# Performance work log

Measured on AMD Instinct MI355X. Metric: run time of the kernel, lower is better.

The kernel has to match this reference:

```python
import jax, jax.numpy as jnp
import numpy as np

B, N, D, DN, F, NUM_F, O, H = 8, 4096, 256, 128, 128, 1024, 8, 1024
EPS = 1e-5

def setup_inputs() -> dict:
    key = jax.random.key(0)
    ks = jax.random.split(key, 10)
    s = 0.02
    x = jax.random.normal(ks[0], (B, N, D), dtype=jnp.float32)
    ctx = jax.random.normal(ks[1], (B, DN), dtype=jnp.float32)
    idx = jax.random.randint(ks[2], (F,), 0, NUM_F, dtype=jnp.int64)
    cond_w = jax.random.normal(ks[3], (DN, 2 * D), dtype=jnp.float32) * s
    cond_b = jnp.zeros((2 * D,), dtype=jnp.float32)
    ffn_w_in = jax.random.normal(ks[4], (D, 2 * H), dtype=jnp.float32) * s
    ffn_b_in = jnp.zeros((2 * H,), dtype=jnp.float32)
    ffn_w_out = jax.random.normal(ks[5], (H, D), dtype=jnp.float32) * s
    ffn_b_out = jnp.zeros((D,), dtype=jnp.float32)
    emb = jax.random.normal(ks[6], (NUM_F, D * O), dtype=jnp.float32) * s
    return {"x": x, "ctx": ctx, "idx": idx, "cond_w": cond_w, "cond_b": cond_b,
            "ffn_w_in": ffn_w_in, "ffn_b_in": ffn_b_in,
            "ffn_w_out": ffn_w_out, "ffn_b_out": ffn_b_out, "emb": emb}

def reference(x, ctx, idx, cond_w, cond_b, ffn_w_in, ffn_b_in, ffn_w_out, ffn_b_out, emb):
    # Conditional LayerNorm: normalize over last dim, FiLM-style modulation from ctx
    mu = jnp.mean(x, axis=-1, keepdims=True)
    var = jnp.mean((x - mu) ** 2, axis=-1, keepdims=True)
    h = (x - mu) * jax.lax.rsqrt(var + EPS)                      # [B,N,D]
    ss = ctx @ cond_w + cond_b                                   # [B,2D]
    scale, shift = jnp.split(ss, 2, axis=-1)                     # [B,D] each
    h = h * (1.0 + scale[:, None, :]) + shift[:, None, :]
    # Gated FFN: in-proj -> (gelu(gate) * value) -> out-proj
    uv = h @ ffn_w_in + ffn_b_in                                 # [B,N,2H]
    u, v = jnp.split(uv, 2, axis=-1)
    y = (jax.nn.gelu(u) * v) @ ffn_w_out + ffn_b_out             # [B,N,D]
    # Embedding-generated per-feature output weights, then batched contraction
    w = emb[idx].reshape(F, D, O)                                # gather [F,D,O]
    out = jnp.einsum('bnd,fdo->bnfo', y, w)                      # [B,N,F,O]
    return out
```

## Files before the change

kernel.cpp:

```cpp
#include <hip/hip_runtime.h>
#include <cstdint>
#include <cstddef>

#define M_TOT 32768
#define D_    256
#define DN_   128
#define TWO_D 512
#define H_    1024
#define TWO_H 2048

typedef unsigned short ushort_t;
typedef __attribute__((ext_vector_type(8))) short bf16x8;
typedef __attribute__((ext_vector_type(4))) float f32x4;

__device__ __forceinline__ ushort_t f2bf(float f) {
  union { float f; uint32_t i; } v; v.f = f;
  uint32_t r = v.i + 0x7fffu + ((v.i >> 16) & 1u);
  return (ushort_t)(r >> 16);
}

__device__ __forceinline__ void async_ld16(const void* g, void* l) {
  __builtin_amdgcn_global_load_lds(
      (const __attribute__((address_space(1))) void*)g,
      (__attribute__((address_space(3))) void*)l, 16, 0, 0);
}

__global__ __launch_bounds__(256) void cond_ss_kernel(
    const float* __restrict__ ctx, const float* __restrict__ cond_w,
    const float* __restrict__ cond_b, float* __restrict__ ss) {
  int j = blockIdx.x * 256 + threadIdx.x;
  int b = j >> 9, col = j & 511;
  float acc = cond_b[col];
  for (int k = 0; k < DN_; ++k)
    acc += ctx[b * DN_ + k] * cond_w[k * TWO_D + col];
  ss[j] = acc;
}

__global__ __launch_bounds__(256) void transpose_f32_bf16_kernel(
    const float* __restrict__ in, ushort_t* __restrict__ out, int R, int C) {
  __shared__ float T[64 * 65];
  int ctiles = C >> 6;
  int bi = blockIdx.x / ctiles, bj = blockIdx.x % ctiles;
  int r0 = bi * 64, c0 = bj * 64;
  int tid = threadIdx.x;
#pragma unroll
  for (int it = 0; it < 16; ++it) {
    int idx = it * 256 + tid;
    int r = idx >> 6, c = idx & 63;
    T[r * 65 + c] = in[(size_t)(r0 + r) * C + c0 + c];
  }
  __syncthreads();
#pragma unroll
  for (int it = 0; it < 8; ++it) {
    int idx = it * 256 + tid;
    int a = idx >> 5;
    int b = (idx & 31) * 2;
    uint32_t pk = (uint32_t)f2bf(T[b * 65 + a]) |
                  ((uint32_t)f2bf(T[(b + 1) * 65 + a]) << 16);
    *(uint32_t*)&out[(size_t)(c0 + a) * R + r0 + b] = pk;
  }
}

__global__ __launch_bounds__(256) void gather_emb_kernel(
    const float* __restrict__ emb, const int* __restrict__ idx,
    ushort_t* __restrict__ W2T) {
  int f = blockIdx.x;
  bool looks64 = (idx[1] == 0) & (idx[3] == 0) & (idx[5] == 0) & (idx[7] == 0);
  int fi = looks64 ? idx[2 * f] : idx[f];
  const float* src = emb + (size_t)fi * 2048;
  int o = threadIdx.x >> 5, d0 = (threadIdx.x & 31) * 8;
  ushort_t buf[8];
#pragma unroll
  for (int k = 0; k < 8; ++k) buf[k] = f2bf(src[(d0 + k) * 8 + o]);
  *(bf16x8*)&W2T[(size_t)(f * 8 + o) * 256 + d0] = *(bf16x8*)buf;
}

__global__ __launch_bounds__(256) void ln_film_kernel(
    const float* __restrict__ x, const float* __restrict__ ss,
    ushort_t* __restrict__ h) {
  int row = blockIdx.x * 4 + (threadIdx.x >> 6);
  int lane = threadIdx.x & 63;
  int b = row >> 12;
  const float* xr = x + (size_t)row * D_;
  float4 pk = *(const float4*)(xr + lane * 4);
  float f0 = pk.x, f1 = pk.y, f2 = pk.z, f3 = pk.w;
  float s = f0 + f1 + f2 + f3;
  float q = f0 * f0 + f1 * f1 + f2 * f2 + f3 * f3;
#pragma unroll
  for (int off = 32; off > 0; off >>= 1) {
    s += __shfl_xor(s, off, 64);
    q += __shfl_xor(q, off, 64);
  }
  float mean = s * (1.0f / 256.0f);
  float var = q * (1.0f / 256.0f) - mean * mean;
  float rs = rsqrtf(var + 1e-5f);
  int d = lane * 4;
  const float* ssb = ss + b * TWO_D;
  float o0 = (f0 - mean) * rs * (1.0f + ssb[d + 0]) + ssb[256 + d + 0];
  float o1 = (f1 - mean) * rs * (1.0f + ssb[d + 1]) + ssb[256 + d + 1];
  float o2 = (f2 - mean) * rs * (1.0f + ssb[d + 2]) + ssb[256 + d + 2];
  float o3 = (f3 - mean) * rs * (1.0f + ssb[d + 3]) + ssb[256 + d + 3];
  uint2 st;
  st.x = (uint32_t)f2bf(o0) | ((uint32_t)f2bf(o1) << 16);
  st.y = (uint32_t)f2bf(o2) | ((uint32_t)f2bf(o3) << 16);
  *(uint2*)(h + (size_t)row * D_ + lane * 4) = st;
}

__global__ __launch_bounds__(256, 2) void ffn_fused_kernel(
    const ushort_t* __restrict__ h,
    const ushort_t* __restrict__ WinT,
    const float* __restrict__ bin,
    const ushort_t* __restrict__ WoutT,
    const float* __restrict__ bout,
    ushort_t* __restrict__ y) {
  __shared__ ushort_t Ah[64 * 256];
  __shared__ ushort_t Sh[64 * 264];
  __shared__ ushort_t Gs[64 * 72];
  const int tid = threadIdx.x, lane = tid & 63, wave = tid >> 6;
  const int r = lane >> 2, q = lane & 3;
  const int l15 = lane & 15, l4 = lane >> 4;
  const int m0 = blockIdx.x * 64;
  const int fragoff = l15 * 32 + l4 * 8;

  for (int t = wave; t < 32; t += 4) {
    int rt = t & 3, kc = t >> 2;
    async_ld16(h + (size_t)(m0 + rt * 16 + r) * 256 + kc * 32 + q * 8, &Ah[t * 512]);
  }

  f32x4 yac[16] = {};

  for (int j = 0; j < 16; ++j) {
    f32x4 uac[4] = {}, vac[4] = {};
#pragma unroll
    for (int s = 0; s < 2; ++s) {
      __syncthreads();
      for (int t = wave; t < 16; t += 4) {
        int rt = t & 3, kc = t >> 2;
        size_t grow = (size_t)(j * 64 + rt * 16 + r);
        async_ld16(WinT + grow * 256 + s * 128 + kc * 32 + q * 8, &Sh[t * 512]);
        async_ld16(WinT + (grow + 1024) * 256 + s * 128 + kc * 32 + q * 8, &Sh[(16 + t) * 512]);
      }
      __syncthreads();
#pragma unroll
      for (int ks = 0; ks < 4; ++ks) {
        bf16x8 af = *(const bf16x8*)&Ah[((s * 4 + ks) * 4 + wave) * 512 + fragoff];
#pragma unroll
        for (int jt = 0; jt < 4; ++jt) {
          bf16x8 bu = *(const bf16x8*)&Sh[(ks * 4 + jt) * 512 + fragoff];
          bf16x8 bv = *(const bf16x8*)&Sh[(16 + ks * 4 + jt) * 512 + fragoff];
          uac[jt] = __builtin_amdgcn_mfma_f32_16x16x32_bf16(af, bu, uac[jt], 0, 0, 0);
          vac[jt] = __builtin_amdgcn_mfma_f32_16x16x32_bf16(af, bv, vac[jt], 0, 0, 0);
        }
      }
    }
#pragma unroll
    for (int jt = 0; jt < 4; ++jt) {
      int col = jt * 16 + l15;
      float bub = bin[j * 64 + col];
      float bvb = bin[1024 + j * 64 + col];
#pragma unroll
      for (int rr = 0; rr < 4; ++rr) {
        float u = uac[jt][rr] + bub;
        float v = vac[jt][rr] + bvb;
        float t = 0.7978845608028654f * (u + 0.044715f * u * u * u);
        float e = __expf(2.0f * t);
        float th = 1.0f - 2.0f / (e + 1.0f);
        float gl = 0.5f * u * (1.0f + th);
        Gs[(wave * 16 + l4 * 4 + rr) * 72 + col] = f2bf(gl * v);
      }
    }
    __syncthreads();
    for (int t = wave; t < 32; t += 4) {
      int nt = t & 15, s2 = t >> 4;
      async_ld16(WoutT + (size_t)(nt * 16 + r) * 1024 + j * 64 + s2 * 32 + q * 8, &Sh[t * 512]);
    }
    __syncthreads();
#pragma unroll
    for (int s2 = 0; s2 < 2; ++s2) {
      bf16x8 gf = *(const bf16x8*)&Gs[(wave * 16 + l15) * 72 + s2 * 32 + l4 * 8];
#pragma unroll
      for (int nt = 0; nt < 16; ++nt) {
        bf16x8 bw = *(const bf16x8*)&Sh[(s2 * 16 + nt) * 512 + fragoff];
        yac[nt] = __builtin_amdgcn_mfma_f32_16x16x32_bf16(gf, bw, yac[nt], 0, 0, 0);
      }
    }
  }
  __syncthreads();
#pragma unroll
  for (int nt = 0; nt < 16; ++nt) {
    int col = nt * 16 + l15;
    float bb = bout[col];
#pragma unroll
    for (int rr = 0; rr < 4; ++rr)
      Sh[(wave * 16 + l4 * 4 + rr) * 264 + col] = f2bf(yac[nt][rr] + bb);
  }
  __syncthreads();
#pragma unroll
  for (int it = 0; it < 8; ++it) {
    int id = it * 256 + tid;
    int rr = id >> 5, cc = id & 31;
    bf16x8 vv = *(const bf16x8*)&Sh[rr * 264 + cc * 8];
    *(bf16x8*)&y[(size_t)(m0 + rr) * 256 + cc * 8] = vv;
  }
}

__global__ __launch_bounds__(256, 2) void gemm_out_kernel(
    const ushort_t* __restrict__ A, const ushort_t* __restrict__ BT,
    float* __restrict__ C) {
  __shared__ ushort_t As[128 * 64];
  __shared__ ushort_t Bs[128 * 64];
  __shared__ float Cs[64 * 132];
  const int tid = threadIdx.x, lane = tid & 63, wave = tid >> 6;
  const int wm = wave >> 1, wn = wave & 1;
  const int m0 = blockIdx.x * 128, n0 = blockIdx.y * 128;
  const int r = lane >> 2, q = lane & 3;
  const int l15 = lane & 15, l4 = lane >> 4;
  const int fragoff = l15 * 32 + l4 * 8;
  const int N = 1024, K = 256;
  f32x4 acc[4][4] = {};
  for (int k0 = 0; k0 < K; k0 += 64) {
    for (int t = wave; t < 16; t += 4) {
      int rt = t >> 1, ks = t & 1;
      async_ld16(A + (size_t)(m0 + rt * 16 + r) * K + k0 + ks * 32 + q * 8, &As[t * 512]);
      async_ld16(BT + (size_t)(n0 + rt * 16 + r) * K + k0 + ks * 32 + q * 8, &Bs[t * 512]);
    }
    __syncthreads();
#pragma unroll
    for (int ks = 0; ks < 2; ++ks) {
      bf16x8 a[4], b[4];
#pragma unroll
      for (int i = 0; i < 4; ++i)
        a[i] = *(const bf16x8*)&As[((wm * 4 + i) * 2 + ks) * 512 + fragoff];
#pragma unroll
      for (int jt = 0; jt < 4; ++jt)
        b[jt] = *(const bf16x8*)&Bs[((wn * 4 + jt) * 2 + ks) * 512 + fragoff];
#pragma unroll
      for (int i = 0; i < 4; ++i)
#pragma unroll
        for (int jt = 0; jt < 4; ++jt)
          acc[i][jt] = __builtin_amdgcn_mfma_f32_16x16x32_bf16(a[i], b[jt], acc[i][jt], 0, 0, 0);
    }
    __syncthreads();
  }
#pragma unroll
  for (int p = 0; p < 2; ++p) {
    __syncthreads();
    if (wm == p) {
#pragma unroll
      for (int jt = 0; jt < 4; ++jt) {
        int col = wn * 64 + jt * 16 + l15;
#pragma unroll
        for (int i = 0; i < 4; ++i) {
          int rl = i * 16 + (l4 << 2);
#pragma unroll
          for (int rr = 0; rr < 4; ++rr)
            Cs[(rl + rr) * 132 + col] = acc[i][jt][rr];
        }
      }
    }
    __syncthreads();
#pragma unroll
    for (int it = 0; it < 8; ++it) {
      int t = it * 256 + tid;
      int rr = t >> 5, c = (t & 31) * 4;
      float4 v = *(const float4*)&Cs[rr * 132 + c];
      *(float4*)&C[(size_t)(m0 + p * 64 + rr) * N + n0 + c] = v;
    }
  }
}

extern "C" void kernel_launch(void* const* d_in, const int* in_sizes, int n_in,
                              void* d_out, int out_size, void* d_ws, size_t ws_size,
                              hipStream_t stream) {
  const float* x      = (const float*)d_in[0];
  const float* ctx    = (const float*)d_in[1];
  const int*   idx    = (const int*)d_in[2];
  const float* cond_w = (const float*)d_in[3];
  const float* cond_b = (const float*)d_in[4];
  const float* w_in   = (const float*)d_in[5];
  const float* b_in   = (const float*)d_in[6];
  const float* w_out  = (const float*)d_in[7];
  const float* b_out  = (const float*)d_in[8];
  const float* emb    = (const float*)d_in[9];

  char* w = (char*)d_ws;
  float* ss = (float*)w;           w += (size_t)8 * TWO_D * 4;
  ushort_t* h = (ushort_t*)w;      w += (size_t)M_TOT * D_ * 2;
  ushort_t* y = (ushort_t*)w;      w += (size_t)M_TOT * D_ * 2;
  ushort_t* WinT = (ushort_t*)w;   w += (size_t)TWO_H * D_ * 2;
  ushort_t* WoutT = (ushort_t*)w;  w += (size_t)D_ * H_ * 2;
  ushort_t* W2T = (ushort_t*)w;    w += (size_t)H_ * D_ * 2;

  cond_ss_kernel<<<16, 256, 0, stream>>>(ctx, cond_w, cond_b, ss);
  transpose_f32_bf16_kernel<<<(D_ / 64) * (TWO_H / 64), 256, 0, stream>>>(w_in, WinT, D_, TWO_H);
  transpose_f32_bf16_kernel<<<(H_ / 64) * (D_ / 64), 256, 0, stream>>>(w_out, WoutT, H_, D_);
  gather_emb_kernel<<<128, 256, 0, stream>>>(emb, idx, W2T);
  ln_film_kernel<<<M_TOT / 4, 256, 0, stream>>>(x, ss, h);
  ffn_fused_kernel<<<M_TOT / 64, 256, 0, stream>>>(h, WinT, b_in, WoutT, b_out, y);
  gemm_out_kernel<<<dim3(M_TOT / 128, H_ / 128), 256, 0, stream>>>(y, W2T, (float*)d_out);
}
```

Baseline: 306.9 us.

## Double-buffer FFN weight tiles in LDS and keep activations in registers

```diff
diff --git a/kernel.cpp b/kernel.cpp
--- a/kernel.cpp
+++ b/kernel.cpp
@@ -113,8 +113,7 @@
     const ushort_t* __restrict__ WoutT,
     const float* __restrict__ bout,
     ushort_t* __restrict__ y) {
-  __shared__ ushort_t Ah[64 * 256];
-  __shared__ ushort_t Sh[64 * 264];
+  __shared__ ushort_t Sh[2][16384];
   __shared__ ushort_t Gs[64 * 72];
   const int tid = threadIdx.x, lane = tid & 63, wave = tid >> 6;
   const int r = lane >> 2, q = lane & 3;
@@ -122,35 +121,94 @@
   const int m0 = blockIdx.x * 64;
   const int fragoff = l15 * 32 + l4 * 8;
 
-  for (int t = wave; t < 32; t += 4) {
-    int rt = t & 3, kc = t >> 2;
-    async_ld16(h + (size_t)(m0 + rt * 16 + r) * 256 + kc * 32 + q * 8, &Ah[t * 512]);
+  const char* winp  = (const char*)WinT  + (wave * 16 + r) * 512 + q * 16;
+  const char* woutp = (const char*)WoutT + (size_t)wave * 32768 + r * 2048 + q * 16;
+
+  const ushort_t* hp = h + (size_t)(m0 + wave * 16 + l15) * 256 + l4 * 8;
+  bf16x8 a_reg[8];
+#pragma unroll
+  for (int kc = 0; kc < 8; ++kc) a_reg[kc] = *(const bf16x8*)(hp + kc * 32);
+
+#pragma unroll
+  for (int i = 0; i < 4; ++i) {
+    int t = i * 4 + wave;
+    async_ld16(winp + i * 64,          &Sh[0][t * 512]);
+    async_ld16(winp + i * 64 + 524288, &Sh[0][(16 + t) * 512]);
   }
 
   f32x4 yac[16] = {};
+  int pb = 0;
 
   for (int j = 0; j < 16; ++j) {
+    const int jb = j * 32768;
     f32x4 uac[4] = {}, vac[4] = {};
-#pragma unroll
-    for (int s = 0; s < 2; ++s) {
-      __syncthreads();
-      for (int t = wave; t < 16; t += 4) {
-        int rt = t & 3, kc = t >> 2;
-        size_t grow = (size_t)(j * 64 + rt * 16 + r);
-        async_ld16(WinT + grow * 256 + s * 128 + kc * 32 + q * 8, &Sh[t * 512]);
-        async_ld16(WinT + (grow + 1024) * 256 + s * 128 + kc * 32 + q * 8, &Sh[(16 + t) * 512]);
-      }
-      __syncthreads();
+
+    asm volatile("s_waitcnt vmcnt(0)" ::: "memory");
+    __builtin_amdgcn_s_barrier();
+    asm volatile("" ::: "memory");
+    {
+      ushort_t* nxt = Sh[pb ^ 1];
+#pragma unroll
+      for (int i = 0; i < 4; ++i) {
+        int t = i * 4 + wave;
+        async_ld16(winp + jb + 256 + i * 64,          &nxt[t * 512]);
+        async_ld16(winp + jb + 256 + i * 64 + 524288, &nxt[(16 + t) * 512]);
+      }
+      const ushort_t* cur = Sh[pb];
+      __builtin_amdgcn_s_setprio(1);
 #pragma unroll
       for (int ks = 0; ks < 4; ++ks) {
-        bf16x8 af = *(const bf16x8*)&Ah[((s * 4 + ks) * 4 + wave) * 512 + fragoff];
+        bf16x8 af = a_reg[ks];
 #pragma unroll
         for (int jt = 0; jt < 4; ++jt) {
-          bf16x8 bu = *(const bf16x8*)&Sh[(ks * 4 + jt) * 512 + fragoff];
-          bf16x8 bv = *(const bf16x8*)&Sh[(16 + ks * 4 + jt) * 512 + fragoff];
+          bf16x8 bu = *(const bf16x8*)&cur[(ks * 4 + jt) * 512 + fragoff];
+          bf16x8 bv = *(const bf16x8*)&cur[(16 + ks * 4 + jt) * 512 + fragoff];
           uac[jt] = __builtin_amdgcn_mfma_f32_16x16x32_bf16(af, bu, uac[jt], 0, 0, 0);
           vac[jt] = __builtin_amdgcn_mfma_f32_16x16x32_bf16(af, bv, vac[jt], 0, 0, 0);
         }
+      }
+      __builtin_amdgcn_s_setprio(0);
+    }
+    pb ^= 1;
+
+    asm volatile("s_waitcnt vmcnt(0)" ::: "memory");
+    __builtin_amdgcn_s_barrier();
+    asm volatile("" ::: "memory");
+    {
+      ushort_t* nxt = Sh[pb ^ 1];
+#pragma unroll
+      for (int i = 0; i < 4; ++i) {
+        int t = i * 4 + wave;
+        async_ld16(woutp + (size_t)i * 131072 + j * 128,      &nxt[t * 512]);
+        async_ld16(woutp + (size_t)i * 131072 + j * 128 + 64, &nxt[(16 + t) * 512]);
+      }
+      const ushort_t* cur = Sh[pb];
+      __builtin_amdgcn_s_setprio(1);
+#pragma unroll
+      for (int ks = 0; ks < 4; ++ks) {
+        bf16x8 af = a_reg[4 + ks];
+#pragma unroll
+        for (int jt = 0; jt < 4; ++jt) {
+          bf16x8 bu = *(const bf16x8*)&cur[(ks * 4 + jt) * 512 + fragoff];
+          bf16x8 bv = *(const bf16x8*)&cur[(16 + ks * 4 + jt) * 512 + fragoff];
+          uac[jt] = __builtin_amdgcn_mfma_f32_16x16x32_bf16(af, bu, uac[jt], 0, 0, 0);
+          vac[jt] = __builtin_amdgcn_mfma_f32_16x16x32_bf16(af, bv, vac[jt], 0, 0, 0);
+        }
+      }
+      __builtin_amdgcn_s_setprio(0);
+    }
+    pb ^= 1;
+
+    asm volatile("s_waitcnt vmcnt(0)" ::: "memory");
+    __builtin_amdgcn_s_barrier();
+    asm volatile("" ::: "memory");
+    if (j < 15) {
+      ushort_t* nxt = Sh[pb ^ 1];
+#pragma unroll
+      for (int i = 0; i < 4; ++i) {
+        int t = i * 4 + wave;
+        async_ld16(winp + jb + 32768 + i * 64,          &nxt[t * 512]);
+        async_ld16(winp + jb + 32768 + i * 64 + 524288, &nxt[(16 + t) * 512]);
       }
     }
 #pragma unroll
@@ -169,37 +227,43 @@
         Gs[(wave * 16 + l4 * 4 + rr) * 72 + col] = f2bf(gl * v);
       }
     }
-    __syncthreads();
-    for (int t = wave; t < 32; t += 4) {
-      int nt = t & 15, s2 = t >> 4;
-      async_ld16(WoutT + (size_t)(nt * 16 + r) * 1024 + j * 64 + s2 * 32 + q * 8, &Sh[t * 512]);
-    }
-    __syncthreads();
-#pragma unroll
-    for (int s2 = 0; s2 < 2; ++s2) {
-      bf16x8 gf = *(const bf16x8*)&Gs[(wave * 16 + l15) * 72 + s2 * 32 + l4 * 8];
-#pragma unroll
-      for (int nt = 0; nt < 16; ++nt) {
-        bf16x8 bw = *(const bf16x8*)&Sh[(s2 * 16 + nt) * 512 + fragoff];
-        yac[nt] = __builtin_amdgcn_mfma_f32_16x16x32_bf16(gf, bw, yac[nt], 0, 0, 0);
-      }
-    }
-  }
-  __syncthreads();
+    {
+      const ushort_t* cur = Sh[pb];
+#pragma unroll
+      for (int s2 = 0; s2 < 2; ++s2) {
+        bf16x8 gf = *(const bf16x8*)&Gs[(wave * 16 + l15) * 72 + s2 * 32 + l4 * 8];
+        __builtin_amdgcn_s_setprio(1);
+#pragma unroll
+        for (int nt = 0; nt < 16; ++nt) {
+          bf16x8 bw = *(const bf16x8*)&cur[(s2 * 16 + nt) * 512 + fragoff];
+          yac[nt] = __builtin_amdgcn_mfma_f32_16x16x32_bf16(gf, bw, yac[nt], 0, 0, 0);
+        }
+        __builtin_amdgcn_s_setprio(0);
+      }
+    }
+    pb ^= 1;
+  }
+
+  asm volatile("s_waitcnt vmcnt(0)" ::: "memory");
+  __builtin_amdgcn_s_barrier();
+  asm volatile("" ::: "memory");
+  ushort_t* E = &Sh[0][0];
 #pragma unroll
   for (int nt = 0; nt < 16; ++nt) {
     int col = nt * 16 + l15;
     float bb = bout[col];
 #pragma unroll
     for (int rr = 0; rr < 4; ++rr)
-      Sh[(wave * 16 + l4 * 4 + rr) * 264 + col] = f2bf(yac[nt][rr] + bb);
-  }
-  __syncthreads();
+      E[(wave * 16 + l4 * 4 + rr) * 264 + col] = f2bf(yac[nt][rr] + bb);
+  }
+  asm volatile("s_waitcnt lgkmcnt(0)" ::: "memory");
+  __builtin_amdgcn_s_barrier();
+  asm volatile("" ::: "memory");
 #pragma unroll
   for (int it = 0; it < 8; ++it) {
     int id = it * 256 + tid;
     int rr = id >> 5, cc = id & 31;
-    bf16x8 vv = *(const bf16x8*)&Sh[rr * 264 + cc * 8];
+    bf16x8 vv = *(const bf16x8*)&E[rr * 264 + cc * 8];
     *(bf16x8*)&y[(size_t)(m0 + rr) * 256 + cc * 8] = vv;
   }
 }
```

Result: faster. 299.1 us (-2.6%).

## Pipeline fused FFN with triple-buffered LDS, register-resident A and swizzled layout

Applied to the files above, without the earlier changes.

```diff
diff --git a/kernel.cpp b/kernel.cpp
--- a/kernel.cpp
+++ b/kernel.cpp
@@ -113,95 +113,172 @@
     const ushort_t* __restrict__ WoutT,
     const float* __restrict__ bout,
     ushort_t* __restrict__ y) {
-  __shared__ ushort_t Ah[64 * 256];
-  __shared__ ushort_t Sh[64 * 264];
+  __shared__ ushort_t S3[3][8192];
   __shared__ ushort_t Gs[64 * 72];
+  __shared__ float Lbin[2048];
   const int tid = threadIdx.x, lane = tid & 63, wave = tid >> 6;
+  const int wm = wave >> 1, wn = wave & 1;
   const int r = lane >> 2, q = lane & 3;
+  const int qs = q ^ ((r >> 1) & 3);
   const int l15 = lane & 15, l4 = lane >> 4;
   const int m0 = blockIdx.x * 64;
-  const int fragoff = l15 * 32 + l4 * 8;
-
-  for (int t = wave; t < 32; t += 4) {
-    int rt = t & 3, kc = t >> 2;
-    async_ld16(h + (size_t)(m0 + rt * 16 + r) * 256 + kc * 32 + q * 8, &Ah[t * 512]);
-  }
-
-  f32x4 yac[16] = {};
+  const int fragoff = l15 * 32 + (l4 ^ ((l15 >> 1) & 3)) * 8;
+
+  const char* winb  = (const char*)WinT  + r * 512 + qs * 16;
+  const char* woutb = (const char*)WoutT + r * 2048 + qs * 16;
+
+  const ushort_t* hp = h + (size_t)(m0 + wm * 32 + l15) * 256 + l4 * 8;
+  bf16x8 a_reg[2][8];
+#pragma unroll
+  for (int rt = 0; rt < 2; ++rt)
+#pragma unroll
+    for (int kc = 0; kc < 8; ++kc)
+      a_reg[rt][kc] = *(const bf16x8*)(hp + rt * 4096 + kc * 32);
+
+#pragma unroll
+  for (int i = 0; i < 2; ++i)
+    async_ld16((const char*)bin + (wave * 2 + i) * 1024 + lane * 16,
+               (char*)Lbin + (wave * 2 + i) * 1024);
+
+  auto stage_in = [&](ushort_t* dst, int jrow, int k0e) {
+#pragma unroll
+    for (int i = 0; i < 4; ++i) {
+      int tt = i * 4 + wave;
+      int vv = tt >> 3, t7 = tt & 7;
+      int ks = t7 >> 2, cc = t7 & 3;
+      async_ld16(winb + (size_t)vv * 524288 + jrow * 32768 + cc * 8192 +
+                     k0e * 2 + ks * 64,
+                 &dst[tt * 512]);
+    }
+  };
+  auto stage_wout = [&](ushort_t* dst, int jrow, int s2) {
+#pragma unroll
+    for (int i = 0; i < 4; ++i) {
+      int tt = i * 4 + wave;
+      async_ld16(woutb + (size_t)tt * 32768 + jrow * 128 + s2 * 64,
+                 &dst[tt * 512]);
+    }
+  };
+
+  stage_in(S3[0], 0, 0);
+  stage_in(S3[1], 0, 64);
+
+  f32x4 yac[2][8] = {};
+
+#define ENTRY4()                                        \
+  asm volatile("s_waitcnt vmcnt(4)" ::: "memory");      \
+  __builtin_amdgcn_s_barrier();                         \
+  asm volatile("" ::: "memory");
+#define ENTRY4L()                                                  \
+  asm volatile("s_waitcnt vmcnt(4) lgkmcnt(0)" ::: "memory");      \
+  __builtin_amdgcn_s_barrier();                                    \
+  asm volatile("" ::: "memory");
+
+#define MFMA_IN(buf, p_)                                                      \
+  {                                                                           \
+    const ushort_t* cur_ = (buf);                                             \
+    __builtin_amdgcn_s_setprio(1);                                            \
+    _Pragma("unroll")                                                         \
+    for (int ks = 0; ks < 2; ++ks) {                                          \
+      _Pragma("unroll")                                                       \
+      for (int jj = 0; jj < 2; ++jj) {                                        \
+        int tt = ks * 4 + wn * 2 + jj;                                        \
+        bf16x8 bu = *(const bf16x8*)&cur_[tt * 512 + fragoff];                \
+        bf16x8 bv = *(const bf16x8*)&cur_[(8 + tt) * 512 + fragoff];          \
+        uac[0][jj] = __builtin_amdgcn_mfma_f32_16x16x32_bf16(a_reg[0][(p_)*2+ks], bu, uac[0][jj], 0, 0, 0); \
+        uac[1][jj] = __builtin_amdgcn_mfma_f32_16x16x32_bf16(a_reg[1][(p_)*2+ks], bu, uac[1][jj], 0, 0, 0); \
+        vac[0][jj] = __builtin_amdgcn_mfma_f32_16x16x32_bf16(a_reg[0][(p_)*2+ks], bv, vac[0][jj], 0, 0, 0); \
+        vac[1][jj] = __builtin_amdgcn_mfma_f32_16x16x32_bf16(a_reg[1][(p_)*2+ks], bv, vac[1][jj], 0, 0, 0); \
+      }                                                                       \
+    }                                                                         \
+    __builtin_amdgcn_s_setprio(0);                                            \
+  }
+
+#define MFMA_OUT(buf, s2_)                                                    \
+  {                                                                           \
+    const ushort_t* cur_ = (buf);                                             \
+    bf16x8 gf0 = *(const bf16x8*)&Gs[(wm * 32 + l15) * 72 + (s2_) * 32 + l4 * 8];      \
+    bf16x8 gf1 = *(const bf16x8*)&Gs[(wm * 32 + 16 + l15) * 72 + (s2_) * 32 + l4 * 8]; \
+    __builtin_amdgcn_s_setprio(1);                                            \
+    _Pragma("unroll")                                                         \
+    for (int nt8 = 0; nt8 < 8; ++nt8) {                                       \
+      bf16x8 bw = *(const bf16x8*)&cur_[(wn * 8 + nt8) * 512 + fragoff];      \
+      yac[0][nt8] = __builtin_amdgcn_mfma_f32_16x16x32_bf16(gf0, bw, yac[0][nt8], 0, 0, 0); \
+      yac[1][nt8] = __builtin_amdgcn_mfma_f32_16x16x32_bf16(gf1, bw, yac[1][nt8], 0, 0, 0); \
+    }                                                                         \
+    __builtin_amdgcn_s_setprio(0);                                            \
+  }
 
   for (int j = 0; j < 16; ++j) {
-    f32x4 uac[4] = {}, vac[4] = {};
-#pragma unroll
-    for (int s = 0; s < 2; ++s) {
-      __syncthreads();
-      for (int t = wave; t < 16; t += 4) {
-        int rt = t & 3, kc = t >> 2;
-        size_t grow = (size_t)(j * 64 + rt * 16 + r);
-        async_ld16(WinT + grow * 256 + s * 128 + kc * 32 + q * 8, &Sh[t * 512]);
-        async_ld16(WinT + (grow + 1024) * 256 + s * 128 + kc * 32 + q * 8, &Sh[(16 + t) * 512]);
-      }
-      __syncthreads();
-#pragma unroll
-      for (int ks = 0; ks < 4; ++ks) {
-        bf16x8 af = *(const bf16x8*)&Ah[((s * 4 + ks) * 4 + wave) * 512 + fragoff];
-#pragma unroll
-        for (int jt = 0; jt < 4; ++jt) {
-          bf16x8 bu = *(const bf16x8*)&Sh[(ks * 4 + jt) * 512 + fragoff];
-          bf16x8 bv = *(const bf16x8*)&Sh[(16 + ks * 4 + jt) * 512 + fragoff];
-          uac[jt] = __builtin_amdgcn_mfma_f32_16x16x32_bf16(af, bu, uac[jt], 0, 0, 0);
-          vac[jt] = __builtin_amdgcn_mfma_f32_16x16x32_bf16(af, bv, vac[jt], 0, 0, 0);
+    const int jn = (j + 1) & 15;
+    f32x4 uac[2][2] = {}, vac[2][2] = {};
+
+    ENTRY4(); stage_in(S3[2], j, 128);  MFMA_IN(S3[0], 0);
+    ENTRY4(); stage_in(S3[0], j, 192);  MFMA_IN(S3[1], 1);
+    ENTRY4(); stage_wout(S3[1], j, 0);  MFMA_IN(S3[2], 2);
+    ENTRY4(); stage_wout(S3[2], j, 1);  MFMA_IN(S3[0], 3);
+
+#pragma unroll
+    for (int jj = 0; jj < 2; ++jj) {
+      int gcol = wn * 32 + jj * 16 + l15;
+      float bub = Lbin[j * 64 + gcol];
+      float bvb = Lbin[1024 + j * 64 + gcol];
+#pragma unroll
+      for (int rt = 0; rt < 2; ++rt) {
+#pragma unroll
+        for (int rr = 0; rr < 4; ++rr) {
+          float u = uac[rt][jj][rr] + bub;
+          float v = vac[rt][jj][rr] + bvb;
+          float t = 0.7978845608028654f * (u + 0.044715f * u * u * u);
+          float e = __expf(2.0f * t);
+          float th = 1.0f - 2.0f / (e + 1.0f);
+          float gl = 0.5f * u * (1.0f + th);
+          Gs[(wm * 32 + rt * 16 + l4 * 4 + rr) * 72 + gcol] = f2bf(gl * v);
         }
       }
     }
-#pragma unroll
-    for (int jt = 0; jt < 4; ++jt) {
-      int col = jt * 16 + l15;
-      float bub = bin[j * 64 + col];
-      float bvb = bin[1024 + j * 64 + col];
-#pragma unroll
-      for (int rr = 0; rr < 4; ++rr) {
-        float u = uac[jt][rr] + bub;
-        float v = vac[jt][rr] + bvb;
-        float t = 0.7978845608028654f * (u + 0.044715f * u * u * u);
-        float e = __expf(2.0f * t);
-        float th = 1.0f - 2.0f / (e + 1.0f);
-        float gl = 0.5f * u * (1.0f + th);
-        Gs[(wave * 16 + l4 * 4 + rr) * 72 + col] = f2bf(gl * v);
+
+    ENTRY4L(); stage_in(S3[0], jn, 0);  MFMA_OUT(S3[1], 0);
+    ENTRY4();  stage_in(S3[1], jn, 64); MFMA_OUT(S3[2], 1);
+  }
+
+  asm volatile("s_waitcnt vmcnt(0)" ::: "memory");
+  __builtin_amdgcn_s_barrier();
+  asm volatile("" ::: "memory");
+  ushort_t* E = &S3[0][0];
+#pragma unroll
+  for (int hh = 0; hh < 2; ++hh) {
+    if (wm == hh) {
+#pragma unroll
+      for (int nt8 = 0; nt8 < 8; ++nt8) {
+        int col = wn * 128 + nt8 * 16 + l15;
+        float bb = bout[col];
+#pragma unroll
+        for (int rt = 0; rt < 2; ++rt)
+#pragma unroll
+          for (int rr = 0; rr < 4; ++rr)
+            E[(rt * 16 + l4 * 4 + rr) * 264 + col] = f2bf(yac[rt][nt8][rr] + bb);
       }
     }
-    __syncthreads();
-    for (int t = wave; t < 32; t += 4) {
-      int nt = t & 15, s2 = t >> 4;
-      async_ld16(WoutT + (size_t)(nt * 16 + r) * 1024 + j * 64 + s2 * 32 + q * 8, &Sh[t * 512]);
-    }
-    __syncthreads();
-#pragma unroll
-    for (int s2 = 0; s2 < 2; ++s2) {
-      bf16x8 gf = *(const bf16x8*)&Gs[(wave * 16 + l15) * 72 + s2 * 32 + l4 * 8];
-#pragma unroll
-      for (int nt = 0; nt < 16; ++nt) {
-        bf16x8 bw = *(const bf16x8*)&Sh[(s2 * 16 + nt) * 512 + fragoff];
-        yac[nt] = __builtin_amdgcn_mfma_f32_16x16x32_bf16(gf, bw, yac[nt], 0, 0, 0);
-      }
-    }
-  }
-  __syncthreads();
-#pragma unroll
-  for (int nt = 0; nt < 16; ++nt) {
-    int col = nt * 16 + l15;
-    float bb = bout[col];
-#pragma unroll
-    for (int rr = 0; rr < 4; ++rr)
-      Sh[(wave * 16 + l4 * 4 + rr) * 264 + col] = f2bf(yac[nt][rr] + bb);
-  }
-  __syncthreads();
-#pragma unroll
-  for (int it = 0; it < 8; ++it) {
-    int id = it * 256 + tid;
-    int rr = id >> 5, cc = id & 31;
-    bf16x8 vv = *(const bf16x8*)&Sh[rr * 264 + cc * 8];
-    *(bf16x8*)&y[(size_t)(m0 + rr) * 256 + cc * 8] = vv;
-  }
+    asm volatile("s_waitcnt lgkmcnt(0)" ::: "memory");
+    __builtin_amdgcn_s_barrier();
+    asm volatile("" ::: "memory");
+#pragma unroll
+    for (int it = 0; it < 4; ++it) {
+      int id = it * 256 + tid;
+      int rr = id >> 5, cc = id & 31;
+      bf16x8 vv = *(const bf16x8*)&E[rr * 264 + cc * 8];
+      *(bf16x8*)&y[(size_t)(m0 + hh * 32 + rr) * 256 + cc * 8] = vv;
+    }
+    if (hh == 0) {
+      __builtin_amdgcn_s_barrier();
+      asm volatile("" ::: "memory");
+    }
+  }
+#undef ENTRY4
+#undef ENTRY4L
+#undef MFMA_IN
+#undef MFMA_OUT
 }
 
 __global__ __launch_bounds__(256, 2) void gemm_out_kernel(
@@ -214,15 +291,16 @@
   const int wm = wave >> 1, wn = wave & 1;
   const int m0 = blockIdx.x * 128, n0 = blockIdx.y * 128;
   const int r = lane >> 2, q = lane & 3;
+  const int qs = q ^ ((r >> 1) & 3);
   const int l15 = lane & 15, l4 = lane >> 4;
-  const int fragoff = l15 * 32 + l4 * 8;
+  const int fragoff = l15 * 32 + (l4 ^ ((l15 >> 1) & 3)) * 8;
   const int N = 1024, K = 256;
   f32x4 acc[4][4] = {};
   for (int k0 = 0; k0 < K; k0 += 64) {
     for (int t = wave; t < 16; t += 4) {
       int rt = t >> 1, ks = t & 1;
-      async_ld16(A + (size_t)(m0 + rt * 16 + r) * K + k0 + ks * 32 + q * 8, &As[t * 512]);
-      async_ld16(BT + (size_t)(n0 + rt * 16 + r) * K + k0 + ks * 32 + q * 8, &Bs[t * 512]);
+      async_ld16(A + (size_t)(m0 + rt * 16 + r) * K + k0 + ks * 32 + qs * 8, &As[t * 512]);
+      async_ld16(BT + (size_t)(n0 + rt * 16 + r) * K + k0 + ks * 32 + qs * 8, &Bs[t * 512]);
     }
     __syncthreads();
 #pragma unroll
```

Measured after the change: 289.4 us. -5.7%, faster.
